# Kernel optimization log

Measured on AMD Instinct MI355X. Metric: run time of the kernel, lower is better.

Reference implementation:

```python
import jax, jax.numpy as jnp
import numpy as np

B, N = 64, 4096

def setup_inputs() -> dict:
    key = jax.random.key(0)
    k1, k2, k3, k4, k5, k6 = jax.random.split(key, 6)
    return {
        "V_mag": jax.random.uniform(k1, (B, N), dtype=jnp.float32, minval=0.9, maxval=1.1),
        "V_ang": 0.3 * jax.random.normal(k2, (B, N), dtype=jnp.float32),
        "P_in": jax.random.normal(k3, (B, N), dtype=jnp.float32),
        "Q_in": jax.random.normal(k4, (B, N), dtype=jnp.float32),
        "G_bus": jax.random.normal(k5, (N, N), dtype=jnp.float32) / np.sqrt(N),
        "B_bus": jax.random.normal(k6, (N, N), dtype=jnp.float32) / np.sqrt(N),
    }

def reference(V_mag, V_ang, P_in, Q_in, G_bus, B_bus):
    # P_i = V_i sum_j V_j (G_ij cos(ti-tj) + B_ij sin(ti-tj))
    # Q_i = V_i sum_j V_j (G_ij sin(ti-tj) - B_ij cos(ti-tj))
    # Angle-addition rewrite (exact): with c_j = V_j cos(t_j), s_j = V_j sin(t_j):
    #   sum_j G_ij V_j cos(ti-tj) = cos(ti)*(G c)_i + sin(ti)*(G s)_i, etc.
    cos_t = jnp.cos(V_ang)  # [B, N]
    sin_t = jnp.sin(V_ang)
    c = V_mag * cos_t       # V_j cos(t_j)
    s = V_mag * sin_t       # V_j sin(t_j)
    Gc = jnp.einsum('ij,bj->bi', G_bus, c)
    Gs = jnp.einsum('ij,bj->bi', G_bus, s)
    Bc = jnp.einsum('ij,bj->bi', B_bus, c)
    Bs = jnp.einsum('ij,bj->bi', B_bus, s)
    # sum_j V_j (G cos + B sin) = cos_ti*(Gc+Bs) + sin_ti*(Gs-Bc)
    P_calc = V_mag * (cos_t * (Gc + Bs) + sin_t * (Gs - Bc))
    # sum_j V_j (G sin - B cos) = sin_ti*(Gc+Bs) - cos_ti*(Gs-Bc)
    Q_calc = V_mag * (sin_t * (Gc + Bs) - cos_t * (Gs - Bc))
    res_P = P_calc - P_in
    res_Q = Q_calc - Q_in
    return (res_P, res_Q)
```

## Files before the change

kernel.cpp:

```cpp
#include <hip/hip_runtime.h>
#include <stdint.h>

#define N_DIM 4096
#define B_DIM 64
#define BN (B_DIM * N_DIM)

typedef __bf16 bf16x8 __attribute__((ext_vector_type(8)));
typedef float floatx4 __attribute__((ext_vector_type(4)));

union FragU { uint4 u; bf16x8 h; };

#define AS1 __attribute__((address_space(1)))
#define AS3 __attribute__((address_space(3)))

__device__ __forceinline__ void gll16(const void* gp, void* lp) {
    __builtin_amdgcn_global_load_lds((const AS1 void*)gp, (AS3 void*)lp, 16, 0, 0);
}

__device__ __forceinline__ unsigned short f2bf_rne(float f) {
    unsigned int u = __float_as_uint(f);
    u += 0x7fffu + ((u >> 16) & 1u);
    return (unsigned short)(u >> 16);
}

__global__ __launch_bounds__(256) void pf_prep(
        const float* __restrict__ Vmag, const float* __restrict__ Vang,
        unsigned short* __restrict__ c_pk, unsigned short* __restrict__ s_pk,
        float* __restrict__ XY) {
    int idx = blockIdx.x * 256 + threadIdx.x;
    int b = idx >> 12;
    int j = idx & 4095;
    float sv, cv;
    sincosf(Vang[idx], &sv, &cv);
    float v = Vmag[idx];
    int p = (((j >> 3) << 6) + b) * 8 + (j & 7);
    c_pk[p] = f2bf_rne(v * cv);
    s_pk[p] = f2bf_rne(v * sv);
    XY[idx] = 0.f;
    XY[idx + BN] = 0.f;
}

#define BUFB 49152
#define ABOFF 16384
#define COFF 32768
#define SOFF 40960
__global__ __launch_bounds__(1024) void pf_gemm(
        const float* __restrict__ G, const float* __restrict__ Bm,
        const unsigned short* __restrict__ c_pk, const unsigned short* __restrict__ s_pk,
        float* __restrict__ XY) {
    __shared__ __align__(16) char lds[2 * BUFB];
    const int tid = threadIdx.x;
    const int wave = tid >> 6;
    const int lane = tid & 63;
    const int n = lane & 15;
    const int quad = lane >> 4;
    const int mt = wave >> 2;
    const int nt = wave & 3;
    const int rb = blockIdx.x & 63;
    const int kq = blockIdx.x >> 6;
    const int i0 = rb << 6;
    const int k0 = kq << 10;

    const int rg = (wave << 2) + (lane >> 4);
    const int gslot = (lane & 15) ^ (rg & 7);
    const float* gsrc = G  + (size_t)(i0 + rg) * N_DIM + k0 + gslot * 4;
    const float* bsrc = Bm + (size_t)(i0 + rg) * N_DIM + k0 + gslot * 4;
    const unsigned short* csbase = (wave < 8) ? c_pk : s_pk;
    const unsigned short* cssrc = csbase + ((size_t)(kq * 128 + (wave & 7)) << 9) + lane * 8;
    char* stgA = lds + wave * 1024;
    char* stgC = lds + COFF + ((wave >= 8) ? (SOFF - COFF) : 0) + (wave & 7) * 1024;

    const int r = (mt << 4) + n;
    const int r7 = n & 7;
    const int arow = r << 8;
    const int csl = ((nt << 4) + n) << 4;

    floatx4 accX = (floatx4){0.f, 0.f, 0.f, 0.f};
    floatx4 accY = (floatx4){0.f, 0.f, 0.f, 0.f};

    gll16(gsrc, stgA);
    gll16(bsrc, stgA + ABOFF);
    gll16(cssrc, stgC);

    for (int ch = 0; ch < 16; ++ch) {
        const int buf = (ch & 1) * BUFB;
        __syncthreads();

        if (ch < 15) {
            const int nb = ((ch + 1) & 1) * BUFB;
            gll16(gsrc + (ch + 1) * 64, stgA + nb);
            gll16(bsrc + (ch + 1) * 64, stgA + nb + ABOFF);
            gll16(cssrc + (size_t)(ch + 1) * 4096, stgC + nb);
        }

        const char* base = lds + buf;
        #pragma unroll
        for (int kk = 0; kk < 2; ++kk) {
            const int u = (kk << 3) + (quad << 1);
            const int s0 = u ^ r7;
            const int s1 = s0 ^ 1;
            float4 g0 = *(const float4*)(base + arow + s0 * 16);
            float4 g1 = *(const float4*)(base + arow + s1 * 16);
            float4 h0 = *(const float4*)(base + ABOFF + arow + s0 * 16);
            float4 h1 = *(const float4*)(base + ABOFF + arow + s1 * 16);
            bf16x8 ag, ah;
            ag[0] = (__bf16)g0.x; ag[1] = (__bf16)g0.y; ag[2] = (__bf16)g0.z; ag[3] = (__bf16)g0.w;
            ag[4] = (__bf16)g1.x; ag[5] = (__bf16)g1.y; ag[6] = (__bf16)g1.z; ag[7] = (__bf16)g1.w;
            ah[0] = (__bf16)h0.x; ah[1] = (__bf16)h0.y; ah[2] = (__bf16)h0.z; ah[3] = (__bf16)h0.w;
            ah[4] = (__bf16)h1.x; ah[5] = (__bf16)h1.y; ah[6] = (__bf16)h1.z; ah[7] = (__bf16)h1.w;

            const int kgo = ((kk << 2) + quad) << 10;
            FragU cf, sf, nf;
            cf.u = *(const uint4*)(base + COFF + kgo + csl);
            sf.u = *(const uint4*)(base + SOFF + kgo + csl);
            nf.u.x = cf.u.x ^ 0x80008000u;
            nf.u.y = cf.u.y ^ 0x80008000u;
            nf.u.z = cf.u.z ^ 0x80008000u;
            nf.u.w = cf.u.w ^ 0x80008000u;

            accX = __builtin_amdgcn_mfma_f32_16x16x32_bf16(ag, cf.h, accX, 0, 0, 0);
            accY = __builtin_amdgcn_mfma_f32_16x16x32_bf16(ah, nf.h, accY, 0, 0, 0);
            accX = __builtin_amdgcn_mfma_f32_16x16x32_bf16(ah, sf.h, accX, 0, 0, 0);
            accY = __builtin_amdgcn_mfma_f32_16x16x32_bf16(ag, sf.h, accY, 0, 0, 0);
        }
    }

    float* Xg = XY;
    float* Yg = XY + BN;
    const int ib = i0 + (mt << 4) + (quad << 2);
    const int bb = (nt << 4) + n;
    #pragma unroll
    for (int rr = 0; rr < 4; ++rr) {
        atomicAdd(Xg + (size_t)bb * N_DIM + ib + rr, accX[rr]);
        atomicAdd(Yg + (size_t)bb * N_DIM + ib + rr, accY[rr]);
    }
}

__global__ __launch_bounds__(256) void pf_epi(
        const float* __restrict__ Vmag, const float* __restrict__ Vang,
        const float* __restrict__ P_in, const float* __restrict__ Q_in,
        const float* __restrict__ XY, float* __restrict__ out) {
    int idx = blockIdx.x * 256 + threadIdx.x;
    float X = XY[idx];
    float Y = XY[idx + BN];
    float sv, cv;
    sincosf(Vang[idx], &sv, &cv);
    float v = Vmag[idx];
    float c = v * cv;
    float s = v * sv;
    out[idx] = c * X + s * Y - P_in[idx];
    out[idx + BN] = s * X - c * Y - Q_in[idx];
}

extern "C" void kernel_launch(void* const* d_in, const int* in_sizes, int n_in,
                              void* d_out, int out_size, void* d_ws, size_t ws_size,
                              hipStream_t stream) {
    const float* Vmag = (const float*)d_in[0];
    const float* Vang = (const float*)d_in[1];
    const float* P_in = (const float*)d_in[2];
    const float* Q_in = (const float*)d_in[3];
    const float* G    = (const float*)d_in[4];
    const float* Bm   = (const float*)d_in[5];
    float* out = (float*)d_out;

    char* ws = (char*)d_ws;
    unsigned short* c_pk = (unsigned short*)(ws);
    unsigned short* s_pk = (unsigned short*)(ws + (512u << 10));
    float* XY = (float*)(ws + (1u << 20));

    hipLaunchKernelGGL(pf_prep, dim3(BN / 256), dim3(256), 0, stream,
                       Vmag, Vang, c_pk, s_pk, XY);
    hipLaunchKernelGGL(pf_gemm, dim3(256), dim3(1024), 0, stream,
                       G, Bm, c_pk, s_pk, XY);
    hipLaunchKernelGGL(pf_epi, dim3(BN / 256), dim3(256), 0, stream,
                       Vmag, Vang, P_in, Q_in, XY, out);
}
```

Baseline: 195.5 us.

## Shrink GEMM blocks to 16 rows and read c/s fragments directly from global

The GEMM block changes from 1024 threads covering 64 rows of G/B to 256 threads covering 16 rows, launched over 1024 blocks with up to 8 blocks per CU. The packed bf16 c/s operands are no longer staged through LDS; each wave loads its fragments straight from global memory, which cuts LDS use to 16 KB per block. The goal is more resident blocks and waves to hide the latency of streaming G/B. In exchange, the c/s vectors are re-read from global/L2 by four times as many blocks, and those loads are not prefetched.

Measured after the change: 197.9 us. About the same (+1.2%).

```diff
diff --git a/kernel.cpp b/kernel.cpp
--- a/kernel.cpp
+++ b/kernel.cpp
@@ -40,11 +40,9 @@
     XY[idx + BN] = 0.f;
 }
 
-#define BUFB 49152
-#define ABOFF 16384
-#define COFF 32768
-#define SOFF 40960
-__global__ __launch_bounds__(1024) void pf_gemm(
+#define BUFB 8192
+#define BOFF 4096
+__global__ __launch_bounds__(256, 8) void pf_gemm(
         const float* __restrict__ G, const float* __restrict__ Bm,
         const unsigned short* __restrict__ c_pk, const unsigned short* __restrict__ s_pk,
         float* __restrict__ XY) {
@@ -54,65 +52,58 @@
     const int lane = tid & 63;
     const int n = lane & 15;
     const int quad = lane >> 4;
-    const int mt = wave >> 2;
-    const int nt = wave & 3;
-    const int rb = blockIdx.x & 63;
-    const int kq = blockIdx.x >> 6;
-    const int i0 = rb << 6;
+    const int rb = blockIdx.x & 255;
+    const int kq = blockIdx.x >> 8;
+    const int i0 = rb << 4;
     const int k0 = kq << 10;
 
-    const int rg = (wave << 2) + (lane >> 4);
-    const int gslot = (lane & 15) ^ (rg & 7);
-    const float* gsrc = G  + (size_t)(i0 + rg) * N_DIM + k0 + gslot * 4;
-    const float* bsrc = Bm + (size_t)(i0 + rg) * N_DIM + k0 + gslot * 4;
-    const unsigned short* csbase = (wave < 8) ? c_pk : s_pk;
-    const unsigned short* cssrc = csbase + ((size_t)(kq * 128 + (wave & 7)) << 9) + lane * 8;
-    char* stgA = lds + wave * 1024;
-    char* stgC = lds + COFF + ((wave >= 8) ? (SOFF - COFF) : 0) + (wave & 7) * 1024;
+    const int sr = (wave << 2) + quad;
+    const int sj = n ^ (sr & 7);
+    const float* gsrc = G  + (size_t)(i0 + sr) * N_DIM + k0 + sj * 4;
+    const float* bsrc = Bm + (size_t)(i0 + sr) * N_DIM + k0 + sj * 4;
+    char* stgG = lds + wave * 1024;
+    char* stgB = lds + BOFF + wave * 1024;
 
-    const int r = (mt << 4) + n;
-    const int r7 = n & 7;
-    const int arow = r << 8;
-    const int csl = ((nt << 4) + n) << 4;
+    const unsigned short* cp0 = c_pk + ((size_t)(kq * 128 + quad) * 64 + (wave << 4) + n) * 8;
+    const unsigned short* sp0 = s_pk + ((size_t)(kq * 128 + quad) * 64 + (wave << 4) + n) * 8;
+
+    const int m7 = n & 7;
+    const int arow = n << 8;
 
     floatx4 accX = (floatx4){0.f, 0.f, 0.f, 0.f};
     floatx4 accY = (floatx4){0.f, 0.f, 0.f, 0.f};
 
-    gll16(gsrc, stgA);
-    gll16(bsrc, stgA + ABOFF);
-    gll16(cssrc, stgC);
+    gll16(gsrc, stgG);
+    gll16(bsrc, stgB);
 
     for (int ch = 0; ch < 16; ++ch) {
         const int buf = (ch & 1) * BUFB;
         __syncthreads();
-
         if (ch < 15) {
             const int nb = ((ch + 1) & 1) * BUFB;
-            gll16(gsrc + (ch + 1) * 64, stgA + nb);
-            gll16(bsrc + (ch + 1) * 64, stgA + nb + ABOFF);
-            gll16(cssrc + (size_t)(ch + 1) * 4096, stgC + nb);
+            gll16(gsrc + (ch + 1) * 64, stgG + nb);
+            gll16(bsrc + (ch + 1) * 64, stgB + nb);
         }
 
         const char* base = lds + buf;
         #pragma unroll
         for (int kk = 0; kk < 2; ++kk) {
-            const int u = (kk << 3) + (quad << 1);
-            const int s0 = u ^ r7;
-            const int s1 = s0 ^ 1;
-            float4 g0 = *(const float4*)(base + arow + s0 * 16);
-            float4 g1 = *(const float4*)(base + arow + s1 * 16);
-            float4 h0 = *(const float4*)(base + ABOFF + arow + s0 * 16);
-            float4 h1 = *(const float4*)(base + ABOFF + arow + s1 * 16);
+            const int s = (kk << 3) + (quad << 1);
+            const int j0 = s ^ m7;
+            const int j1 = (s + 1) ^ m7;
+            float4 g0 = *(const float4*)(base + arow + j0 * 16);
+            float4 g1 = *(const float4*)(base + arow + j1 * 16);
+            float4 h0 = *(const float4*)(base + BOFF + arow + j0 * 16);
+            float4 h1 = *(const float4*)(base + BOFF + arow + j1 * 16);
             bf16x8 ag, ah;
             ag[0] = (__bf16)g0.x; ag[1] = (__bf16)g0.y; ag[2] = (__bf16)g0.z; ag[3] = (__bf16)g0.w;
             ag[4] = (__bf16)g1.x; ag[5] = (__bf16)g1.y; ag[6] = (__bf16)g1.z; ag[7] = (__bf16)g1.w;
             ah[0] = (__bf16)h0.x; ah[1] = (__bf16)h0.y; ah[2] = (__bf16)h0.z; ah[3] = (__bf16)h0.w;
             ah[4] = (__bf16)h1.x; ah[5] = (__bf16)h1.y; ah[6] = (__bf16)h1.z; ah[7] = (__bf16)h1.w;
 
-            const int kgo = ((kk << 2) + quad) << 10;
             FragU cf, sf, nf;
-            cf.u = *(const uint4*)(base + COFF + kgo + csl);
-            sf.u = *(const uint4*)(base + SOFF + kgo + csl);
+            cf.u = *(const uint4*)(cp0 + (size_t)ch * 4096 + kk * 2048);
+            sf.u = *(const uint4*)(sp0 + (size_t)ch * 4096 + kk * 2048);
             nf.u.x = cf.u.x ^ 0x80008000u;
             nf.u.y = cf.u.y ^ 0x80008000u;
             nf.u.z = cf.u.z ^ 0x80008000u;
@@ -127,8 +118,8 @@
 
     float* Xg = XY;
     float* Yg = XY + BN;
-    const int ib = i0 + (mt << 4) + (quad << 2);
-    const int bb = (nt << 4) + n;
+    const int ib = i0 + (quad << 2);
+    const int bb = (wave << 4) + n;
     #pragma unroll
     for (int rr = 0; rr < 4; ++rr) {
         atomicAdd(Xg + (size_t)bb * N_DIM + ib + rr, accX[rr]);
@@ -170,7 +161,7 @@
 
     hipLaunchKernelGGL(pf_prep, dim3(BN / 256), dim3(256), 0, stream,
                        Vmag, Vang, c_pk, s_pk, XY);
-    hipLaunchKernelGGL(pf_gemm, dim3(256), dim3(1024), 0, stream,
+    hipLaunchKernelGGL(pf_gemm, dim3(1024), dim3(256), 0, stream,
                        G, Bm, c_pk, s_pk, XY);
     hipLaunchKernelGGL(pf_epi, dim3(BN / 256), dim3(256), 0, stream,
                        Vmag, Vang, P_in, Q_in, XY, out);
```
